# Performance work log

Measured on AMD Instinct MI355X. Metric: run time of the kernel, lower is better.

## Reference

```python
import jax, jax.numpy as jnp
import numpy as np
from jax import lax

VOCAB, EMB, HID = 50000, 1024, 1024
H2 = HID // 2            # per-direction LSTM hidden
T = 4096                 # sequence length
NTAGS, START, STOP = 5, 3, 4
NEG = -10000.0


def setup_inputs() -> dict:
    key = jax.random.key(0)
    ks = jax.random.split(key, 16)
    n = lambda i, shape, s=0.05: (jax.random.normal(ks[i], shape) * s).astype(jnp.float32)
    inp = {
        "sentence": jax.random.randint(ks[0], (T,), 0, VOCAB, dtype=jnp.int64 if jax.config.jax_enable_x64 else jnp.int32),
        "h0": jax.random.normal(ks[1], (2, H2), jnp.float32),
        "c0": jax.random.normal(ks[2], (2, H2), jnp.float32),
        "embed": jax.random.normal(ks[3], (VOCAB, EMB), jnp.float32),
        "Wih_f": n(4, (4 * H2, EMB)), "Whh_f": n(5, (4 * H2, H2)),
        "bih_f": n(6, (4 * H2,)),     "bhh_f": n(7, (4 * H2,)),
        "Wih_b": n(8, (4 * H2, EMB)), "Whh_b": n(9, (4 * H2, H2)),
        "bih_b": n(10, (4 * H2,)),    "bhh_b": n(11, (4 * H2,)),
        "Wout": n(12, (NTAGS, HID)),  "bout": n(13, (NTAGS,)),
    }
    trans = jax.random.normal(ks[14], (NTAGS, NTAGS), jnp.float32)
    trans = trans.at[START, :].set(NEG).at[:, STOP].set(NEG)
    inp["trans"] = trans
    return inp


def _lstm_dir(xs, h0, c0, Wih, Whh, bih, bhh):
    # torch LSTM gate order: i, f, g, o
    def step(carry, x):
        h, c = carry
        g = Wih @ x + bih + Whh @ h + bhh
        i, f, gg, o = jnp.split(g, 4)
        c = jax.nn.sigmoid(f) * c + jax.nn.sigmoid(i) * jnp.tanh(gg)
        h = jax.nn.sigmoid(o) * jnp.tanh(c)
        return (h, c), h
    _, hs = lax.scan(step, (h0, c0), xs)
    return hs  # [T, H2]


def reference(sentence, h0, c0, embed,
              Wih_f, Whh_f, bih_f, bhh_f,
              Wih_b, Whh_b, bih_b, bhh_b,
              Wout, bout, trans):
    xs = embed[sentence]  # [T, EMB]
    hf = _lstm_dir(xs, h0[0], c0[0], Wih_f, Whh_f, bih_f, bhh_f)
    hb = _lstm_dir(xs[::-1], h0[1], c0[1], Wih_b, Whh_b, bih_b, bhh_b)[::-1]
    feats = jnp.concatenate([hf, hb], axis=-1) @ Wout.T + bout  # [T, NTAGS]

    # Viterbi decode
    fv0 = jnp.full((NTAGS,), NEG, jnp.float32).at[START].set(0.0)

    def vstep(fv, feat):
        scores = fv[None, :] + trans            # [next_tag, prev_tag]
        bp = jnp.argmax(scores, axis=1)         # best prev for each next
        fv_new = jnp.max(scores, axis=1) + feat
        return fv_new, bp

    fv, bptrs = lax.scan(vstep, fv0, feats)     # bptrs: [T, NTAGS]
    terminal = fv + trans[STOP]
    best = jnp.argmax(terminal)
    path_score = terminal[best]

    def back(tag, bp):
        prev = bp[tag]
        return prev, prev
    _, path_rev = lax.scan(back, best, bptrs[::-1])  # tags at t=T-1..0, last is START
    full = jnp.concatenate([best[None], path_rev])    # length T+1
    best_path = full[::-1][1:]                        # drop START, forward order, length T
    return path_score, best_path
```

## Files before the change

kernel.cpp:

```cpp
#include <hip/hip_runtime.h>
#include <math.h>

#define VOCAB 50000
#define EMB   1024
#define H2    512
#define R4    2048
#define TLEN  4096
#define NTAGS 5
#define STARTT 3
#define STOPT  4
#define NEGV  (-10000.0f)

#define DWG   32
#define SLICE 16

typedef unsigned long long u64;

#define ALOAD64(p)    __hip_atomic_load((p), __ATOMIC_RELAXED, __HIP_MEMORY_SCOPE_AGENT)
#define ASTORE64(p,v) __hip_atomic_store((p), (v), __ATOMIC_RELAXED, __HIP_MEMORY_SCOPE_AGENT)

__device__ __forceinline__ float fsig(float x) {
    return __builtin_amdgcn_rcpf(1.f + __expf(-x));
}
__device__ __forceinline__ float ftanh(float x) {
    return 1.f - 2.f * __builtin_amdgcn_rcpf(1.f + __expf(2.f * x));
}

__global__ __launch_bounds__(256) void input_gemm(
    const int* __restrict__ sent, const float* __restrict__ embed,
    const float* __restrict__ WihF, const float* __restrict__ WihB,
    const float* __restrict__ bihF, const float* __restrict__ bhhF,
    const float* __restrict__ bihB, const float* __restrict__ bhhB,
    float* __restrict__ G)
{
    __shared__ float As[32 * 64];
    __shared__ float Bs[32 * 64];
    const int tid = threadIdx.x;
    const int tm = blockIdx.x * 64;
    const int tn = blockIdx.y * 64;
    const int dir = blockIdx.z;
    const float* Wih = dir ? WihB : WihF;

    const int lr = tid >> 2;
    const int lp = tid & 3;
    const int srow = sent[tm + lr];
    const float* arow = embed + (size_t)srow * EMB;
    const float* brow = Wih + (size_t)(tn + lr) * EMB;

    const int mt = (tid & 15) * 4;
    const int nt = (tid >> 4) * 4;
    float acc[4][4] = {};

    for (int k0 = 0; k0 < EMB; k0 += 32) {
        float4 a0 = *(const float4*)(arow + k0 + lp * 8);
        float4 a1 = *(const float4*)(arow + k0 + lp * 8 + 4);
        float4 b0 = *(const float4*)(brow + k0 + lp * 8);
        float4 b1 = *(const float4*)(brow + k0 + lp * 8 + 4);
        __syncthreads();
        const int kb = lp * 8;
        As[(kb + 0) * 64 + lr] = a0.x; As[(kb + 1) * 64 + lr] = a0.y;
        As[(kb + 2) * 64 + lr] = a0.z; As[(kb + 3) * 64 + lr] = a0.w;
        As[(kb + 4) * 64 + lr] = a1.x; As[(kb + 5) * 64 + lr] = a1.y;
        As[(kb + 6) * 64 + lr] = a1.z; As[(kb + 7) * 64 + lr] = a1.w;
        Bs[(kb + 0) * 64 + lr] = b0.x; Bs[(kb + 1) * 64 + lr] = b0.y;
        Bs[(kb + 2) * 64 + lr] = b0.z; Bs[(kb + 3) * 64 + lr] = b0.w;
        Bs[(kb + 4) * 64 + lr] = b1.x; Bs[(kb + 5) * 64 + lr] = b1.y;
        Bs[(kb + 6) * 64 + lr] = b1.z; Bs[(kb + 7) * 64 + lr] = b1.w;
        __syncthreads();
        #pragma unroll
        for (int k = 0; k < 32; ++k) {
            float4 av = *(const float4*)(As + k * 64 + mt);
            float4 bv = *(const float4*)(Bs + k * 64 + nt);
            acc[0][0] += av.x * bv.x; acc[0][1] += av.x * bv.y; acc[0][2] += av.x * bv.z; acc[0][3] += av.x * bv.w;
            acc[1][0] += av.y * bv.x; acc[1][1] += av.y * bv.y; acc[1][2] += av.y * bv.z; acc[1][3] += av.y * bv.w;
            acc[2][0] += av.z * bv.x; acc[2][1] += av.z * bv.y; acc[2][2] += av.z * bv.z; acc[2][3] += av.z * bv.w;
            acc[3][0] += av.w * bv.x; acc[3][1] += av.w * bv.y; acc[3][2] += av.w * bv.z; acc[3][3] += av.w * bv.w;
        }
    }

    const float* bih = dir ? bihB : bihF;
    const float* bhh = dir ? bhhB : bhhF;
    float4 bias;
    bias.x = bih[tn + nt + 0] + bhh[tn + nt + 0];
    bias.y = bih[tn + nt + 1] + bhh[tn + nt + 1];
    bias.z = bih[tn + nt + 2] + bhh[tn + nt + 2];
    bias.w = bih[tn + nt + 3] + bhh[tn + nt + 3];
    float* Gd = G + (size_t)dir * TLEN * R4;
    #pragma unroll
    for (int ii = 0; ii < 4; ++ii) {
        float4 o;
        o.x = acc[ii][0] + bias.x; o.y = acc[ii][1] + bias.y;
        o.z = acc[ii][2] + bias.z; o.w = acc[ii][3] + bias.w;
        *(float4*)(Gd + (size_t)(tm + mt + ii) * R4 + tn + nt) = o;
    }
}

__global__ __launch_bounds__(256, 1) void lstm_rec(
    const float* __restrict__ WhhF, const float* __restrict__ WhhB,
    const float* __restrict__ h0, const float* __restrict__ c0,
    const float* __restrict__ G, float* __restrict__ hs,
    u64* hbuf)
{
    const int tid  = threadIdx.x;
    const int dir  = blockIdx.x >> 5;
    const int wg   = blockIdx.x & 31;
    const int base = wg * SLICE;
    const int wave = tid >> 6;
    const int wl   = tid & 63;
    const int e_loc = wl >> 4;
    const int gp    = (wl >> 3) & 1;
    const int qs    = wl & 7;
    const int e     = wave * 4 + e_loc;
    const int grow0 = gp * H2 + base + e;
    const int grow1 = (gp + 2) * H2 + base + e;
    const bool prod = (wl & 15) == 0;
    const float* Whh = dir ? WhhB : WhhF;

    float4 W0[16], W1[16];
    {
        const float4* s0 = (const float4*)(Whh + (size_t)grow0 * H2 + qs * 64);
        const float4* s1 = (const float4*)(Whh + (size_t)grow1 * H2 + qs * 64);
        #pragma unroll
        for (int j = 0; j < 16; ++j) { W0[j] = s0[j]; W1[j] = s1[j]; }
    }

    __shared__ float hsh[8 * 68];

    u64* hb = hbuf + (size_t)dir * 2 * H2;
    float cc = 0.f;
    if (prod) {
        cc = c0[dir * H2 + base + e];
        float hv = h0[dir * H2 + base + e];
        u64 pack = ((u64)1u << 32) | (u64)__float_as_uint(hv);
        ASTORE64(hb + base + e, pack);
    }

    const float* Gd = G + (size_t)dir * TLEN * R4;
    float* hsd = hs + (size_t)dir * TLEN * H2;

    for (int s = 0; s < TLEN; ++s) {
        const int t = dir ? (TLEN - 1 - s) : s;
        const float* gptr = Gd + (size_t)t * R4;
        float gva = gptr[grow0];
        float gvb = gptr[grow1];

        const unsigned want = (unsigned)(s + 1);
        u64* src = hb + (s & 1) * H2 + tid * 2;
        u64 v0 = ALOAD64(src);
        u64 v1 = ALOAD64(src + 1);
        while ((unsigned)(v0 >> 32) != want || (unsigned)(v1 >> 32) != want) {
            v0 = ALOAD64(src);
            v1 = ALOAD64(src + 1);
        }

        {
            int i0 = tid * 2;
            int seg = i0 >> 6, idx = i0 & 63;
            hsh[seg * 68 + idx]     = __uint_as_float((unsigned)v0);
            hsh[seg * 68 + idx + 1] = __uint_as_float((unsigned)v1);
        }
        __syncthreads();

        const float4* hq = (const float4*)(hsh + qs * 68);
        float p00 = 0.f, p01 = 0.f, p02 = 0.f, p03 = 0.f;
        float p10 = 0.f, p11 = 0.f, p12 = 0.f, p13 = 0.f;
        #pragma unroll
        for (int j = 0; j < 16; ++j) {
            float4 h4 = hq[j];
            p00 += W0[j].x * h4.x; p01 += W0[j].y * h4.y;
            p02 += W0[j].z * h4.z; p03 += W0[j].w * h4.w;
            p10 += W1[j].x * h4.x; p11 += W1[j].y * h4.y;
            p12 += W1[j].z * h4.z; p13 += W1[j].w * h4.w;
        }
        float t0 = (p00 + p01) + (p02 + p03);
        float t1 = (p10 + p11) + (p12 + p13);
        t0 += __shfl_xor(t0, 1); t0 += __shfl_xor(t0, 2); t0 += __shfl_xor(t0, 4);
        t1 += __shfl_xor(t1, 1); t1 += __shfl_xor(t1, 2); t1 += __shfl_xor(t1, 4);
        t0 += gva;
        t1 += gvb;

        const int lb = wl & 48;
        float pf = __shfl(t0, lb + 8);
        float po = __shfl(t1, lb + 8);

        if (prod) {
            float i_ = fsig(t0);
            float f_ = fsig(pf);
            float g_ = ftanh(t1);
            float o_ = fsig(po);
            cc = f_ * cc + i_ * g_;
            float hn = o_ * ftanh(cc);
            u64 pack = ((u64)(unsigned)(s + 2) << 32) | (u64)__float_as_uint(hn);
            ASTORE64(hb + ((s + 1) & 1) * H2 + base + e, pack);
            hsd[(size_t)t * H2 + base + e] = hn;
        }
        __syncthreads();
    }
}

__global__ __launch_bounds__(64) void feat_kernel(
    const float* __restrict__ hs, const float* __restrict__ Wout,
    const float* __restrict__ bout, float* __restrict__ feats)
{
    const int t = blockIdx.x;
    const int lane = threadIdx.x;
    const float* hf = hs + (size_t)t * H2;
    const float* hb = hs + (size_t)TLEN * H2 + (size_t)t * H2;
    float x[16];
    #pragma unroll
    for (int r = 0; r < 8; ++r) x[r] = hf[lane + r * 64];
    #pragma unroll
    for (int r = 0; r < 8; ++r) x[8 + r] = hb[lane + r * 64];
    for (int j = 0; j < NTAGS; ++j) {
        const float* wr = Wout + (size_t)j * EMB;
        float p = 0.f;
        #pragma unroll
        for (int r = 0; r < 8; ++r) p += x[r] * wr[lane + r * 64];
        #pragma unroll
        for (int r = 0; r < 8; ++r) p += x[8 + r] * wr[H2 + lane + r * 64];
        #pragma unroll
        for (int off = 32; off > 0; off >>= 1) p += __shfl_down(p, off);
        if (lane == 0) feats[t * NTAGS + j] = p + bout[j];
    }
}

__global__ __launch_bounds__(64) void viterbi_kernel(
    const float* __restrict__ feats, const float* __restrict__ trans,
    float* __restrict__ out)
{
    __shared__ unsigned bp[TLEN];
    __shared__ float fch[256 * NTAGS];
    const int lane = threadIdx.x;
    const bool act = lane < 25;
    const int j = act ? (lane / 5) : 0;
    const int i = act ? (lane % 5) : 0;
    const int j5 = j * 5;
    const float tji = act ? trans[j * 5 + i] : -1e30f;
    float fv = (i == STARTT) ? 0.f : NEGV;

    for (int c0 = 0; c0 < TLEN; c0 += 256) {
        __syncthreads();
        for (int m = lane; m < 256 * NTAGS; m += 64) fch[m] = feats[c0 * NTAGS + m];
        __syncthreads();
        for (int tt = 0; tt < 256; ++tt) {
            float score = fv + tji;
            float v0 = __shfl(score, j5 + 0);
            float v1 = __shfl(score, j5 + 1);
            float v2 = __shfl(score, j5 + 2);
            float v3 = __shfl(score, j5 + 3);
            float v4 = __shfl(score, j5 + 4);
            float mm = v0; int mi = 0;
            if (v1 > mm) { mm = v1; mi = 1; }
            if (v2 > mm) { mm = v2; mi = 2; }
            if (v3 > mm) { mm = v3; mi = 3; }
            if (v4 > mm) { mm = v4; mi = 4; }
            float fnew = mm + fch[tt * NTAGS + j];
            unsigned word = ((unsigned)__shfl(mi, 0)  & 7u)
                          | (((unsigned)__shfl(mi, 5)  & 7u) << 3)
                          | (((unsigned)__shfl(mi, 10) & 7u) << 6)
                          | (((unsigned)__shfl(mi, 15) & 7u) << 9)
                          | (((unsigned)__shfl(mi, 20) & 7u) << 12);
            if (lane == 0) bp[c0 + tt] = word;
            fv = __shfl(fnew, i * 5);
        }
    }
    __syncthreads();

    float tstop = (lane < 5) ? trans[STOPT * 5 + lane] : -1e30f;
    float term = fv + tstop;
    float b0 = __shfl(term, 0), b1 = __shfl(term, 1), b2 = __shfl(term, 2);
    float b3 = __shfl(term, 3), b4 = __shfl(term, 4);
    float bsc = b0; int best = 0;
    if (b1 > bsc) { bsc = b1; best = 1; }
    if (b2 > bsc) { bsc = b2; best = 2; }
    if (b3 > bsc) { bsc = b3; best = 3; }
    if (b4 > bsc) { bsc = b4; best = 4; }

    if (lane == 0) {
        out[0] = bsc;
        int tag = best;
        out[TLEN] = (float)tag;
        #pragma unroll 16
        for (int t = TLEN - 1; t >= 1; --t) {
            tag = (int)((bp[t] >> (3 * tag)) & 7u);
            out[t] = (float)tag;
        }
    }
}

extern "C" void kernel_launch(void* const* d_in, const int* in_sizes, int n_in,
                              void* d_out, int out_size, void* d_ws, size_t ws_size,
                              hipStream_t stream) {
    const int*   sent  = (const int*)d_in[0];
    const float* h0    = (const float*)d_in[1];
    const float* c0    = (const float*)d_in[2];
    const float* embed = (const float*)d_in[3];
    const float* Wih_f = (const float*)d_in[4];
    const float* Whh_f = (const float*)d_in[5];
    const float* bih_f = (const float*)d_in[6];
    const float* bhh_f = (const float*)d_in[7];
    const float* Wih_b = (const float*)d_in[8];
    const float* Whh_b = (const float*)d_in[9];
    const float* bih_b = (const float*)d_in[10];
    const float* bhh_b = (const float*)d_in[11];
    const float* Wout  = (const float*)d_in[12];
    const float* bout  = (const float*)d_in[13];
    const float* trans = (const float*)d_in[14];

    char* ws = (char*)d_ws;
    float*    G     = (float*)(ws);
    float*    hs    = (float*)(ws + 67108864);
    u64*      hbuf  = (u64*)(ws + 83886080);
    float*    feats = (float*)(ws + 83918848);

    input_gemm<<<dim3(TLEN / 64, R4 / 64, 2), 256, 0, stream>>>(
        sent, embed, Wih_f, Wih_b, bih_f, bhh_f, bih_b, bhh_b, G);
    lstm_rec<<<2 * DWG, 256, 0, stream>>>(Whh_f, Whh_b, h0, c0, G, hs, hbuf);
    feat_kernel<<<TLEN, 64, 0, stream>>>(hs, Wout, bout, feats);
    viterbi_kernel<<<1, 64, 0, stream>>>(feats, trans, (float*)d_out);
}
```

Before: 8.915 ms.

## Double-buffer LSTM recurrence shared state, prefetch gate inputs, batch hidden-state stores

The recurrent LSTM kernel now keeps two shared-memory buffers for the incoming hidden vector, which removes the trailing barrier in each timestep. It unrolls the loop by four so the precomputed input-gate values can be prefetched two steps ahead. Hidden outputs are collected in shared memory and written out as float4 stores every 64 steps instead of one scalar global store per step. The spin-wait polls now use s_sleep, and the handshake buffer is zeroed with a memset before launch. Dropping the second barrier relies on parity-based flag sequencing to stay race-free, and the sleep may add latency to the critical-path handoff between steps.

```diff
diff --git a/kernel.cpp b/kernel.cpp
--- a/kernel.cpp
+++ b/kernel.cpp
@@ -1,5 +1,6 @@
 #include <hip/hip_runtime.h>
 #include <math.h>
+#include <stddef.h>
 
 #define VOCAB 50000
 #define EMB   1024
@@ -124,7 +125,8 @@
         for (int j = 0; j < 16; ++j) { W0[j] = s0[j]; W1[j] = s1[j]; }
     }
 
-    __shared__ float hsh[8 * 68];
+    __shared__ float hsh[2][8 * 68];
+    __shared__ float hs_acc[64][16];
 
     u64* hb = hbuf + (size_t)dir * 2 * H2;
     float cc = 0.f;
@@ -137,65 +139,96 @@
 
     const float* Gd = G + (size_t)dir * TLEN * R4;
     float* hsd = hs + (size_t)dir * TLEN * H2;
-
-    for (int s = 0; s < TLEN; ++s) {
-        const int t = dir ? (TLEN - 1 - s) : s;
-        const float* gptr = Gd + (size_t)t * R4;
-        float gva = gptr[grow0];
-        float gvb = gptr[grow1];
-
-        const unsigned want = (unsigned)(s + 1);
-        u64* src = hb + (s & 1) * H2 + tid * 2;
-        u64 v0 = ALOAD64(src);
-        u64 v1 = ALOAD64(src + 1);
-        while ((unsigned)(v0 >> 32) != want || (unsigned)(v1 >> 32) != want) {
-            v0 = ALOAD64(src);
-            v1 = ALOAD64(src + 1);
+    const ptrdiff_t sstep = dir ? -(ptrdiff_t)R4 : (ptrdiff_t)R4;
+    const float* g0p = Gd + (size_t)(dir ? TLEN - 1 : 0) * R4;
+
+    u64* srcP0 = hb + tid * 2;
+    u64* srcP1 = hb + H2 + tid * 2;
+
+    float gA0 = g0p[grow0], gA1 = g0p[grow1];
+    float gB0 = (g0p + sstep)[grow0], gB1 = (g0p + sstep)[grow1];
+    float gC0, gC1, gD0, gD1;
+
+#define STEP(S, PAR, GC0_, GC1_, GN0_, GN1_, SNEXT)                           \
+  {                                                                           \
+      \
+    const unsigned want = (unsigned)((S) + 1);                                \
+    u64* src = (PAR) ? srcP1 : srcP0;                                         \
+    u64 v0 = ALOAD64(src);                                                    \
+    u64 v1 = ALOAD64(src + 1);                                                \
+    while ((unsigned)(v0 >> 32) != want) {                                    \
+        __builtin_amdgcn_s_sleep(1); v0 = ALOAD64(src);                       \
+    }                                                                         \
+    while ((unsigned)(v1 >> 32) != want) {                                    \
+        __builtin_amdgcn_s_sleep(1); v1 = ALOAD64(src + 1);                   \
+    }                                                                         \
+    {                                                                         \
+        int i0 = tid * 2;                                                     \
+        int seg = i0 >> 6, idx = i0 & 63;                                     \
+        hsh[PAR][seg * 68 + idx]     = __uint_as_float((unsigned)v0);         \
+        hsh[PAR][seg * 68 + idx + 1] = __uint_as_float((unsigned)v1);         \
+    }                                                                         \
+    __syncthreads();                                                          \
+           \
+    {                                                                         \
+        const float* gn = g0p + (ptrdiff_t)(SNEXT) * sstep;                   \
+        GN0_ = gn[grow0]; GN1_ = gn[grow1];                                   \
+    }                                                                         \
+                                \
+    const float4* hq = (const float4*)(&hsh[PAR][qs * 68]);                   \
+    float p00 = 0.f, p01 = 0.f, p02 = 0.f, p03 = 0.f;                         \
+    float p10 = 0.f, p11 = 0.f, p12 = 0.f, p13 = 0.f;                         \
+    _Pragma("unroll")                                                         \
+    for (int j = 0; j < 16; ++j) {                                            \
+        float4 h4 = hq[j];                                                    \
+        p00 += W0[j].x * h4.x; p01 += W0[j].y * h4.y;                         \
+        p02 += W0[j].z * h4.z; p03 += W0[j].w * h4.w;                         \
+        p10 += W1[j].x * h4.x; p11 += W1[j].y * h4.y;                         \
+        p12 += W1[j].z * h4.z; p13 += W1[j].w * h4.w;                         \
+    }                                                                         \
+    float t0 = (p00 + p01) + (p02 + p03);                                     \
+    float t1 = (p10 + p11) + (p12 + p13);                                     \
+    t0 += __shfl_xor(t0, 1); t0 += __shfl_xor(t0, 2); t0 += __shfl_xor(t0, 4);\
+    t1 += __shfl_xor(t1, 1); t1 += __shfl_xor(t1, 2); t1 += __shfl_xor(t1, 4);\
+    t0 += GC0_;                              \
+    t1 += GC1_;                                                               \
+    const int lb = wl & 48;                                                   \
+    float pf = __shfl(t0, lb + 8);                            \
+    float po = __shfl(t1, lb + 8);                            \
+    if (prod) {                                                               \
+        float i_ = fsig(t0);                                                  \
+        float f_ = fsig(pf);                                                  \
+        float g_ = ftanh(t1);                                                 \
+        float o_ = fsig(po);                                                  \
+        cc = f_ * cc + i_ * g_;                                               \
+        float hn = o_ * ftanh(cc);                                            \
+        u64 pack = ((u64)(unsigned)((S) + 2) << 32) | (u64)__float_as_uint(hn); \
+        ASTORE64(hb + (1 - (PAR)) * H2 + base + e, pack);                     \
+        hs_acc[(S) & 63][e] = hn;              \
+    }                                                                         \
+       \
+       \
+  }
+
+    for (int s = 0; s < TLEN; s += 4) {
+        const int n2 = s + 2;
+        const int n3 = s + 3;
+        const int n4 = (s + 4 < TLEN) ? s + 4 : TLEN - 1;
+        const int n5 = (s + 5 < TLEN) ? s + 5 : TLEN - 1;
+        STEP(s,     0, gA0, gA1, gC0, gC1, n2);
+        STEP(s + 1, 1, gB0, gB1, gD0, gD1, n3);
+        STEP(s + 2, 0, gC0, gC1, gA0, gA1, n4);
+        STEP(s + 3, 1, gD0, gD1, gB0, gB1, n5);
+        if ((s & 63) == 60) {
+            __syncthreads();
+            const int sb = tid >> 2, q = tid & 3;
+            const int ss = (s - 60) + sb;
+            const int t = dir ? (TLEN - 1 - ss) : ss;
+            float4 val = *(const float4*)(&hs_acc[sb][q * 4]);
+            *(float4*)(hsd + (size_t)t * H2 + base + q * 4) = val;
         }
-
-        {
-            int i0 = tid * 2;
-            int seg = i0 >> 6, idx = i0 & 63;
-            hsh[seg * 68 + idx]     = __uint_as_float((unsigned)v0);
-            hsh[seg * 68 + idx + 1] = __uint_as_float((unsigned)v1);
-        }
-        __syncthreads();
-
-        const float4* hq = (const float4*)(hsh + qs * 68);
-        float p00 = 0.f, p01 = 0.f, p02 = 0.f, p03 = 0.f;
-        float p10 = 0.f, p11 = 0.f, p12 = 0.f, p13 = 0.f;
-        #pragma unroll
-        for (int j = 0; j < 16; ++j) {
-            float4 h4 = hq[j];
-            p00 += W0[j].x * h4.x; p01 += W0[j].y * h4.y;
-            p02 += W0[j].z * h4.z; p03 += W0[j].w * h4.w;
-            p10 += W1[j].x * h4.x; p11 += W1[j].y * h4.y;
-            p12 += W1[j].z * h4.z; p13 += W1[j].w * h4.w;
-        }
-        float t0 = (p00 + p01) + (p02 + p03);
-        float t1 = (p10 + p11) + (p12 + p13);
-        t0 += __shfl_xor(t0, 1); t0 += __shfl_xor(t0, 2); t0 += __shfl_xor(t0, 4);
-        t1 += __shfl_xor(t1, 1); t1 += __shfl_xor(t1, 2); t1 += __shfl_xor(t1, 4);
-        t0 += gva;
-        t1 += gvb;
-
-        const int lb = wl & 48;
-        float pf = __shfl(t0, lb + 8);
-        float po = __shfl(t1, lb + 8);
-
-        if (prod) {
-            float i_ = fsig(t0);
-            float f_ = fsig(pf);
-            float g_ = ftanh(t1);
-            float o_ = fsig(po);
-            cc = f_ * cc + i_ * g_;
-            float hn = o_ * ftanh(cc);
-            u64 pack = ((u64)(unsigned)(s + 2) << 32) | (u64)__float_as_uint(hn);
-            ASTORE64(hb + ((s + 1) & 1) * H2 + base + e, pack);
-            hsd[(size_t)t * H2 + base + e] = hn;
-        }
-        __syncthreads();
-    }
+    }
+#undef STEP
 }
 
 __global__ __launch_bounds__(64) void feat_kernel(
@@ -313,6 +346,8 @@
     u64*      hbuf  = (u64*)(ws + 83886080);
     float*    feats = (float*)(ws + 83918848);
 
+    hipMemsetAsync(hbuf, 0, 2 * 2 * H2 * sizeof(u64), stream);
+
     input_gemm<<<dim3(TLEN / 64, R4 / 64, 2), 256, 0, stream>>>(
         sent, embed, Wih_f, Wih_b, bih_f, bhh_f, bih_b, bhh_b, G);
     lstm_rec<<<2 * DWG, 256, 0, stream>>>(Whh_f, Whh_b, h0, c0, G, hs, hbuf);
```

New measurement: 11.35 ms. 1.27x slower.
